# Optimization experiments

Hardware: AMD Instinct MI355X
Metric: run time of the kernel (lower is better)

Reference implementation:

```python
import jax, jax.numpy as jnp
import numpy as np

VOCAB, EMB, HID, T, B, NCLS = 50000, 300, 512, 128, 256, 3


def _lstm_final_h(x, lens, W, b):
    """TF BasicLSTMCell semantics (gate order i,j,f,o; forget_bias=1.0) with
    dynamic_rnn sequence_length masking; returns final hidden state [B, HID].
    x: [B, T, EMB] float, lens: [B] int, W: [EMB+HID, 4*HID], b: [4*HID].
    """
    xt = jnp.swapaxes(x, 0, 1)                       # [T, B, EMB]
    mask = jnp.arange(T)[:, None] < lens[None, :]    # [T, B]

    def step(carry, inp):
        c, h = carry
        x_t, m = inp
        z = jnp.concatenate([x_t, h], axis=-1) @ W + b   # [B, 4*HID]
        i, j, f, o = jnp.split(z, 4, axis=-1)
        c_new = c * jax.nn.sigmoid(f + 1.0) + jax.nn.sigmoid(i) * jnp.tanh(j)
        h_new = jnp.tanh(c_new) * jax.nn.sigmoid(o)
        m = m[:, None]
        return (jnp.where(m, c_new, c), jnp.where(m, h_new, h)), None

    init = (jnp.zeros((x.shape[0], HID), x.dtype),
            jnp.zeros((x.shape[0], HID), x.dtype))
    (c, h), _ = jax.lax.scan(step, init, (xt, mask))
    return h


def setup_inputs() -> dict:
    key = jax.random.key(0)
    ks = jax.random.split(key, 12)
    s = 0.05
    return {
        "left_ids": jax.random.randint(ks[0], (B, T), 0, VOCAB, dtype=jnp.int32),
        "right_ids": jax.random.randint(ks[1], (B, T), 0, VOCAB, dtype=jnp.int32),
        "left_len": jax.random.randint(ks[2], (B,), 1, T + 1, dtype=jnp.int32),
        "right_len": jax.random.randint(ks[3], (B,), 1, T + 1, dtype=jnp.int32),
        "embeddings": jax.random.normal(ks[4], (VOCAB, EMB), jnp.float32) * s,
        "W_l": jax.random.normal(ks[5], (EMB + HID, 4 * HID), jnp.float32) * s,
        "b_l": jnp.zeros((4 * HID,), jnp.float32),
        "W_r": jax.random.normal(ks[6], (EMB + HID, 4 * HID), jnp.float32) * s,
        "b_r": jnp.zeros((4 * HID,), jnp.float32),
        "W_d": jax.random.normal(ks[7], (2 * HID, NCLS), jnp.float32) * s,
        "b_d": jnp.zeros((NCLS,), jnp.float32),
    }


def reference(left_ids, right_ids, left_len, right_len,
              embeddings, W_l, b_l, W_r, b_r, W_d, b_d):
    left_x = embeddings[left_ids]      # [B, T, EMB]
    right_x = embeddings[right_ids]    # [B, T, EMB]
    h_l = _lstm_final_h(left_x, left_len, W_l, b_l)     # [B, HID]
    h_r = _lstm_final_h(right_x, right_len, W_r, b_r)   # [B, HID]
    logits = jnp.concatenate([h_l, h_r], axis=1) @ W_d + b_d  # [B, NCLS]
    return logits
```

## Files before the change

### kernel.cpp

```cpp
#include <hip/hip_runtime.h>


using bf16x8 = __attribute__((ext_vector_type(8))) __bf16;
using f32x4  = __attribute__((ext_vector_type(4))) float;
using u32x4  = __attribute__((ext_vector_type(4))) unsigned int;
typedef unsigned short u16;
typedef unsigned long long u64;

#define NT 128
#define ROWB 1664
#define SWZ(row, off) ((off) ^ (((row) & 7) << 4))

#define LGKM0  asm volatile("s_waitcnt lgkmcnt(0)" ::: "memory")
#define VM0    asm volatile("s_waitcnt vmcnt(0)" ::: "memory")
#define BAR()  __builtin_amdgcn_s_barrier()
#define SCHED0 __builtin_amdgcn_sched_barrier(0)

__device__ __forceinline__ u16 f2bf(float f) {
  union { float f; unsigned u; } v; v.f = f;
  unsigned r = v.u + 0x7fffu + ((v.u >> 16) & 1u);
  return (u16)(r >> 16);
}
__device__ __forceinline__ float sigf(float x) { return 1.f / (1.f + __expf(-x)); }
__device__ __forceinline__ float tanhf_(float x) { return 2.f / (1.f + __expf(-2.f * x)) - 1.f; }

__device__ __forceinline__ void setA26(bf16x8 (&A)[26], int kt, bf16x8 v) {
  switch (kt) {
    case 0:A[0]=v;break;  case 1:A[1]=v;break;  case 2:A[2]=v;break;
    case 3:A[3]=v;break;  case 4:A[4]=v;break;  case 5:A[5]=v;break;
    case 6:A[6]=v;break;  case 7:A[7]=v;break;  case 8:A[8]=v;break;
    case 9:A[9]=v;break;  case 10:A[10]=v;break; case 11:A[11]=v;break;
    case 12:A[12]=v;break; case 13:A[13]=v;break; case 14:A[14]=v;break;
    case 15:A[15]=v;break; case 16:A[16]=v;break; case 17:A[17]=v;break;
    case 18:A[18]=v;break; case 19:A[19]=v;break; case 20:A[20]=v;break;
    case 21:A[21]=v;break; case 22:A[22]=v;break; case 23:A[23]=v;break;
    case 24:A[24]=v;break; case 25:A[25]=v;break;
  }
}

__global__ __launch_bounds__(256, 1) void lstm_persist(
    const int* __restrict__ lids, const int* __restrict__ rids,
    const int* __restrict__ llen, const int* __restrict__ rlen,
    const float* __restrict__ emb,
    const float* __restrict__ Wl, const float* __restrict__ bl,
    const float* __restrict__ Wr, const float* __restrict__ br,
    u64* __restrict__ hbuf,
    float* __restrict__ hfin,
    unsigned int* __restrict__ bar)
{
  __shared__ __align__(16) unsigned char sB[32 * ROWB];
  __shared__ __align__(8)  u16 sH[32][36];
  __shared__ int sI[4096];

  const int tid = threadIdx.x;
  const int w = tid >> 6, l = tid & 63;
  const int bid = blockIdx.x;
  const int xcd = bid & 7, idx = bid >> 3;
  const int grp = xcd * 2 + (idx >> 4);
  const int ct  = idx & 15;
  const int lstm = grp >> 3, bt = grp & 7;
  const int b0 = bt * 32, u0 = ct * 32;

  const int*   ids  = lstm ? rids : lids;
  const int*   lenp = lstm ? rlen : llen;
  const float* W    = lstm ? Wr : Wl;
  const float* bv   = lstm ? br : bl;

  bf16x8 A0[26], A1[26];
  {
    float* sW = (float*)sB;
    for (int kc = 0; kc < 13; ++kc) {
      for (int i = 0; i < 32; ++i) {
        int id2 = tid + i * 256;
        int c = id2 & 31, r = (id2 >> 5) & 63, g = id2 >> 11;
        int kk = kc * 64 + r;
        float v = 0.f;
        if (kk < 300)       v = W[kk * 2048 + g * 512 + u0 + c];
        else if (kk >= 320) v = W[(kk - 20) * 2048 + g * 512 + u0 + c];
        sW[(g * 64 + r) * 32 + c] = v;
      }
      __syncthreads();
      #pragma unroll
      for (int kt2 = 0; kt2 < 2; ++kt2) {
        int kt = kc * 2 + kt2;
        #pragma unroll
        for (int mf2 = 0; mf2 < 2; ++mf2) {
          int mf = w * 2 + mf2;
          int rho = mf * 16 + (l & 15);
          int du = rho >> 2, g = rho & 3;
          union { u16 s[8]; bf16x8 v; } tmp;
          #pragma unroll
          for (int j = 0; j < 8; ++j) {
            int kr = kt2 * 32 + ((l >> 4) << 3) + j;
            tmp.s[j] = f2bf(sW[(g * 64 + kr) * 32 + du]);
          }
          if (mf2 == 0) setA26(A0, kt, tmp.v); else setA26(A1, kt, tmp.v);
        }
      }
      __syncthreads();
    }
  }

  if (tid < 160) {
    int row = tid / 5, c5 = tid - (tid / 5) * 5;
    *(u64*)(sB + row * ROWB + SWZ(row, 600 + c5 * 8)) = 0ULL;
  }
  {
    const int* src = ids + b0 * NT;
    #pragma unroll
    for (int i = 0; i < 4; ++i)
      *(int4*)&sI[(tid + i * 256) * 4] = *(const int4*)&src[(tid + i * 256) * 4];
  }
  __syncthreads();

  int ldsoff[10], sirow[10], foff[10];
  #pragma unroll
  for (int i = 0; i < 10; ++i) {
    int id2 = tid + i * 256;
    int row = id2 / 75, f4 = id2 - row * 75;
    ldsoff[i] = row * ROWB + SWZ(row, f4 * 8);
    sirow[i]  = row * NT;
    foff[i]   = f4 * 4;
  }
  int hoff[16];
  #pragma unroll
  for (int i = 0; i < 16; ++i) {
    int id2 = tid + i * 256;
    int row = id2 >> 7, c8 = id2 & 127;
    hoff[i] = row * ROWB + SWZ(row, 640 + c8 * 8);
  }

  int lenn[2];
  lenn[0] = lenp[b0 + (l & 15)];
  lenn[1] = lenp[b0 + 16 + (l & 15)];
  float bia[2][4];
  #pragma unroll
  for (int mf2 = 0; mf2 < 2; ++mf2) {
    int du = w * 8 + mf2 * 4 + (l >> 4);
    #pragma unroll
    for (int g = 0; g < 4; ++g) bia[mf2][g] = bv[g * 512 + u0 + du];
  }
  float cst[2][2] = {{0.f, 0.f}, {0.f, 0.f}};
  float hst[2][2] = {{0.f, 0.f}, {0.f, 0.f}};

  float4 px[10];
  #pragma unroll
  for (int i = 0; i < 10; ++i)
    if (i < 9 || tid < 96) {
      int eid = sI[sirow[i]];
      px[i] = *(const float4*)(emb + eid * 300 + foff[i]);
    }

  const int r0 = l & 15, r1 = 16 + (l & 15);

  for (int t = 0; t < NT; ++t) {
    u64 hld[16];
    const u64* hsrc = hbuf + (((lstm * 2 + ((t & 1) ^ 1)) * 256) + b0) * 128;
    #pragma unroll
    for (int i = 0; i < 16; ++i) {
      u64 v = 0ULL;
      if (t > 0)
        v = __hip_atomic_load(&hsrc[tid + i * 256], __ATOMIC_RELAXED,
                              __HIP_MEMORY_SCOPE_AGENT);
      hld[i] = v;
    }
    #pragma unroll
    for (int i = 0; i < 10; ++i)
      if (i < 9 || tid < 96) {
        float4 xv = px[i];
        u64 pk = (u64)f2bf(xv.x) | ((u64)f2bf(xv.y) << 16) |
                 ((u64)f2bf(xv.z) << 32) | ((u64)f2bf(xv.w) << 48);
        *(u64*)(sB + ldsoff[i]) = pk;
      }
    {
      int tn = (t + 1) & (NT - 1);
      #pragma unroll
      for (int i = 0; i < 10; ++i)
        if (i < 9 || tid < 96) {
          int eid = sI[sirow[i] + tn];
          px[i] = *(const float4*)(emb + eid * 300 + foff[i]);
        }
    }
    #pragma unroll
    for (int i = 0; i < 16; ++i) *(u64*)(sB + hoff[i]) = hld[i];

    LGKM0; BAR(); SCHED0;

    f32x4 acc[2][2];
    acc[0][0] = {0.f,0.f,0.f,0.f}; acc[0][1] = {0.f,0.f,0.f,0.f};
    acc[1][0] = {0.f,0.f,0.f,0.f}; acc[1][1] = {0.f,0.f,0.f,0.f};
    #pragma unroll
    for (int kt = 0; kt < 26; ++kt) {
      int kb = kt * 64 + ((l >> 4) << 4);
      bf16x8 B0 = __builtin_bit_cast(bf16x8, *(const u32x4*)(sB + r0 * ROWB + SWZ(r0, kb)));
      bf16x8 B1 = __builtin_bit_cast(bf16x8, *(const u32x4*)(sB + r1 * ROWB + SWZ(r1, kb)));
      acc[0][0] = __builtin_amdgcn_mfma_f32_16x16x32_bf16(A0[kt], B0, acc[0][0], 0, 0, 0);
      acc[0][1] = __builtin_amdgcn_mfma_f32_16x16x32_bf16(A0[kt], B1, acc[0][1], 0, 0, 0);
      acc[1][0] = __builtin_amdgcn_mfma_f32_16x16x32_bf16(A1[kt], B0, acc[1][0], 0, 0, 0);
      acc[1][1] = __builtin_amdgcn_mfma_f32_16x16x32_bf16(A1[kt], B1, acc[1][1], 0, 0, 0);
    }

    #pragma unroll
    for (int mf2 = 0; mf2 < 2; ++mf2)
      #pragma unroll
      for (int n = 0; n < 2; ++n) {
        f32x4 z = acc[mf2][n];
        float zi = z[0] + bia[mf2][0];
        float zj = z[1] + bia[mf2][1];
        float zf = z[2] + bia[mf2][2];
        float zo = z[3] + bia[mf2][3];
        float cn = cst[mf2][n] * sigf(zf + 1.f) + sigf(zi) * tanhf_(zj);
        float hn = tanhf_(cn) * sigf(zo);
        if (t < lenn[n]) { cst[mf2][n] = cn; hst[mf2][n] = hn; }
        sH[n * 16 + (l & 15)][w * 8 + mf2 * 4 + (l >> 4)] = f2bf(hst[mf2][n]);
      }
    LGKM0; BAR(); SCHED0;

    {
      int bbL = tid >> 3, u8 = tid & 7;
      u64 pk = *(const u64*)&sH[bbL][u8 * 4];
      u64* hdst = hbuf + (((lstm * 2 + (t & 1)) * 256) + b0 + bbL) * 128 + (u0 >> 2) + u8;
      __hip_atomic_store(hdst, pk, __ATOMIC_RELAXED, __HIP_MEMORY_SCOPE_AGENT);
    }
    VM0; BAR();

    if (tid == 0) {
      __hip_atomic_fetch_add(&bar[grp * 32], 1u, __ATOMIC_RELAXED,
                             __HIP_MEMORY_SCOPE_AGENT);
      unsigned target = 16u * (unsigned)(t + 1);
      while (__hip_atomic_load(&bar[grp * 32], __ATOMIC_RELAXED,
                               __HIP_MEMORY_SCOPE_AGENT) < target)
        __builtin_amdgcn_s_sleep(1);
    }
    BAR(); SCHED0;
  }

  #pragma unroll
  for (int mf2 = 0; mf2 < 2; ++mf2)
    #pragma unroll
    for (int n = 0; n < 2; ++n) {
      int bb = b0 + n * 16 + (l & 15);
      int uu = u0 + w * 8 + mf2 * 4 + (l >> 4);
      hfin[lstm * (256 * 512) + bb * 512 + uu] = hst[mf2][n];
    }
}

__global__ void dense_out(const float* __restrict__ hfin,
                          const float* __restrict__ Wd, const float* __restrict__ bd,
                          float* __restrict__ out) {
  const int b = blockIdx.x, l = threadIdx.x;
  float a0 = 0.f, a1 = 0.f, a2 = 0.f;
  for (int i = l; i < 1024; i += 64) {
    float hv = (i < 512) ? hfin[b * 512 + i] : hfin[256 * 512 + b * 512 + (i - 512)];
    a0 += hv * Wd[i * 3 + 0];
    a1 += hv * Wd[i * 3 + 1];
    a2 += hv * Wd[i * 3 + 2];
  }
  #pragma unroll
  for (int off = 32; off > 0; off >>= 1) {
    a0 += __shfl_down(a0, off);
    a1 += __shfl_down(a1, off);
    a2 += __shfl_down(a2, off);
  }
  if (l == 0) {
    out[b * 3 + 0] = a0 + bd[0];
    out[b * 3 + 1] = a1 + bd[1];
    out[b * 3 + 2] = a2 + bd[2];
  }
}

extern "C" void kernel_launch(void* const* d_in, const int* in_sizes, int n_in,
                              void* d_out, int out_size, void* d_ws, size_t ws_size,
                              hipStream_t stream) {
  const int*   lids = (const int*)d_in[0];
  const int*   rids = (const int*)d_in[1];
  const int*   llen = (const int*)d_in[2];
  const int*   rlen = (const int*)d_in[3];
  const float* emb  = (const float*)d_in[4];
  const float* Wl   = (const float*)d_in[5];
  const float* bl   = (const float*)d_in[6];
  const float* Wr   = (const float*)d_in[7];
  const float* br   = (const float*)d_in[8];
  const float* Wd   = (const float*)d_in[9];
  const float* bd   = (const float*)d_in[10];

  unsigned char* ws = (unsigned char*)d_ws;
  unsigned int* bar = (unsigned int*)ws;
  u64*   hbuf = (u64*)(ws + 4096);
  float* hfin = (float*)(ws + 4096 + (1u << 20));

  hipMemsetAsync(bar, 0, 2048, stream);
  hipLaunchKernelGGL(lstm_persist, dim3(256), dim3(256), 0, stream,
                     lids, rids, llen, rlen, emb, Wl, bl, Wr, br, hbuf, hfin, bar);
  hipLaunchKernelGGL(dense_out, dim3(256), dim3(64), 0, stream,
                     hfin, Wd, bd, (float*)d_out);
}
```

Baseline: 718.7 us.

## Overlap input-projection MFMAs with cross-block barrier wait in LSTM recurrence

Splits the per-step gate GEMM into the input part (k-tiles 0-9) and the recurrent part (k-tiles 10-25). After publishing h and signalling the inter-block counter, each block computes the next step's input contribution and prefetches embeddings two steps ahead, and only then waits on the barrier. This moves x-projection work and the embedding staging off the serial critical path between steps. It skips the h load and recurrent MFMAs at t=0, and splits the barrier into an arrive after the store and a wait at the start of the next step, which needs careful ordering of the LDS reuse of the x region.

```diff
diff --git a/kernel.cpp b/kernel.cpp
--- a/kernel.cpp
+++ b/kernel.cpp
@@ -65,6 +65,7 @@
   const int*   lenp = lstm ? rlen : llen;
   const float* W    = lstm ? Wr : Wl;
   const float* bv   = lstm ? br : bl;
+  unsigned int* const blp = bar + grp * 32;
 
   bf16x8 A0[26], A1[26];
   {
@@ -111,7 +112,6 @@
     for (int i = 0; i < 4; ++i)
       *(int4*)&sI[(tid + i * 256) * 4] = *(const int4*)&src[(tid + i * 256) * 4];
   }
-  __syncthreads();
 
   int ldsoff[10], sirow[10], foff[10];
   #pragma unroll
@@ -142,69 +142,76 @@
   }
   float cst[2][2] = {{0.f, 0.f}, {0.f, 0.f}};
   float hst[2][2] = {{0.f, 0.f}, {0.f, 0.f}};
+  __syncthreads();
 
   float4 px[10];
   #pragma unroll
   for (int i = 0; i < 10; ++i)
     if (i < 9 || tid < 96) {
       int eid = sI[sirow[i]];
+      float4 xv = *(const float4*)(emb + eid * 300 + foff[i]);
+      u64 pk = (u64)f2bf(xv.x) | ((u64)f2bf(xv.y) << 16) |
+               ((u64)f2bf(xv.z) << 32) | ((u64)f2bf(xv.w) << 48);
+      *(u64*)(sB + ldsoff[i]) = pk;
+    }
+  #pragma unroll
+  for (int i = 0; i < 10; ++i)
+    if (i < 9 || tid < 96) {
+      int eid = sI[sirow[i] + 1];
       px[i] = *(const float4*)(emb + eid * 300 + foff[i]);
     }
+  __syncthreads();
 
   const int r0 = l & 15, r1 = 16 + (l & 15);
 
+  f32x4 xacc[2][2];
+  xacc[0][0] = {0.f,0.f,0.f,0.f}; xacc[0][1] = {0.f,0.f,0.f,0.f};
+  xacc[1][0] = {0.f,0.f,0.f,0.f}; xacc[1][1] = {0.f,0.f,0.f,0.f};
+  #pragma unroll
+  for (int kt = 0; kt < 10; ++kt) {
+    int kb = kt * 64 + ((l >> 4) << 4);
+    bf16x8 B0 = __builtin_bit_cast(bf16x8, *(const u32x4*)(sB + r0 * ROWB + SWZ(r0, kb)));
+    bf16x8 B1 = __builtin_bit_cast(bf16x8, *(const u32x4*)(sB + r1 * ROWB + SWZ(r1, kb)));
+    xacc[0][0] = __builtin_amdgcn_mfma_f32_16x16x32_bf16(A0[kt], B0, xacc[0][0], 0, 0, 0);
+    xacc[0][1] = __builtin_amdgcn_mfma_f32_16x16x32_bf16(A0[kt], B1, xacc[0][1], 0, 0, 0);
+    xacc[1][0] = __builtin_amdgcn_mfma_f32_16x16x32_bf16(A1[kt], B0, xacc[1][0], 0, 0, 0);
+    xacc[1][1] = __builtin_amdgcn_mfma_f32_16x16x32_bf16(A1[kt], B1, xacc[1][1], 0, 0, 0);
+  }
+
   for (int t = 0; t < NT; ++t) {
-    u64 hld[16];
-    const u64* hsrc = hbuf + (((lstm * 2 + ((t & 1) ^ 1)) * 256) + b0) * 128;
-    #pragma unroll
-    for (int i = 0; i < 16; ++i) {
-      u64 v = 0ULL;
-      if (t > 0)
-        v = __hip_atomic_load(&hsrc[tid + i * 256], __ATOMIC_RELAXED,
-                              __HIP_MEMORY_SCOPE_AGENT);
-      hld[i] = v;
-    }
-    #pragma unroll
-    for (int i = 0; i < 10; ++i)
-      if (i < 9 || tid < 96) {
-        float4 xv = px[i];
-        u64 pk = (u64)f2bf(xv.x) | ((u64)f2bf(xv.y) << 16) |
-                 ((u64)f2bf(xv.z) << 32) | ((u64)f2bf(xv.w) << 48);
-        *(u64*)(sB + ldsoff[i]) = pk;
-      }
-    {
-      int tn = (t + 1) & (NT - 1);
-      #pragma unroll
-      for (int i = 0; i < 10; ++i)
-        if (i < 9 || tid < 96) {
-          int eid = sI[sirow[i] + tn];
-          px[i] = *(const float4*)(emb + eid * 300 + foff[i]);
-        }
-    }
-    #pragma unroll
-    for (int i = 0; i < 16; ++i) *(u64*)(sB + hoff[i]) = hld[i];
-
-    LGKM0; BAR(); SCHED0;
-
-    f32x4 acc[2][2];
-    acc[0][0] = {0.f,0.f,0.f,0.f}; acc[0][1] = {0.f,0.f,0.f,0.f};
-    acc[1][0] = {0.f,0.f,0.f,0.f}; acc[1][1] = {0.f,0.f,0.f,0.f};
-    #pragma unroll
-    for (int kt = 0; kt < 26; ++kt) {
-      int kb = kt * 64 + ((l >> 4) << 4);
-      bf16x8 B0 = __builtin_bit_cast(bf16x8, *(const u32x4*)(sB + r0 * ROWB + SWZ(r0, kb)));
-      bf16x8 B1 = __builtin_bit_cast(bf16x8, *(const u32x4*)(sB + r1 * ROWB + SWZ(r1, kb)));
-      acc[0][0] = __builtin_amdgcn_mfma_f32_16x16x32_bf16(A0[kt], B0, acc[0][0], 0, 0, 0);
-      acc[0][1] = __builtin_amdgcn_mfma_f32_16x16x32_bf16(A0[kt], B1, acc[0][1], 0, 0, 0);
-      acc[1][0] = __builtin_amdgcn_mfma_f32_16x16x32_bf16(A1[kt], B0, acc[1][0], 0, 0, 0);
-      acc[1][1] = __builtin_amdgcn_mfma_f32_16x16x32_bf16(A1[kt], B1, acc[1][1], 0, 0, 0);
+    if (t > 0) {
+      if (tid == 0) {
+        unsigned target = 16u * (unsigned)t;
+        while (__hip_atomic_load(blp, __ATOMIC_RELAXED, __HIP_MEMORY_SCOPE_AGENT) < target)
+          __builtin_amdgcn_s_sleep(1);
+      }
+      BAR(); SCHED0;
+      const u64* hsrc = hbuf + (((lstm * 2 + ((t & 1) ^ 1)) * 256) + b0) * 128;
+      u64 hld[16];
+      #pragma unroll
+      for (int i = 0; i < 16; ++i)
+        hld[i] = __hip_atomic_load(&hsrc[tid + i * 256], __ATOMIC_RELAXED,
+                                   __HIP_MEMORY_SCOPE_AGENT);
+      #pragma unroll
+      for (int i = 0; i < 16; ++i) *(u64*)(sB + hoff[i]) = hld[i];
+      LGKM0; BAR(); SCHED0;
+      #pragma unroll
+      for (int kt = 10; kt < 26; ++kt) {
+        int kb = kt * 64 + ((l >> 4) << 4);
+        bf16x8 B0 = __builtin_bit_cast(bf16x8, *(const u32x4*)(sB + r0 * ROWB + SWZ(r0, kb)));
+        bf16x8 B1 = __builtin_bit_cast(bf16x8, *(const u32x4*)(sB + r1 * ROWB + SWZ(r1, kb)));
+        xacc[0][0] = __builtin_amdgcn_mfma_f32_16x16x32_bf16(A0[kt], B0, xacc[0][0], 0, 0, 0);
+        xacc[0][1] = __builtin_amdgcn_mfma_f32_16x16x32_bf16(A0[kt], B1, xacc[0][1], 0, 0, 0);
+        xacc[1][0] = __builtin_amdgcn_mfma_f32_16x16x32_bf16(A1[kt], B0, xacc[1][0], 0, 0, 0);
+        xacc[1][1] = __builtin_amdgcn_mfma_f32_16x16x32_bf16(A1[kt], B1, xacc[1][1], 0, 0, 0);
+      }
     }
 
     #pragma unroll
     for (int mf2 = 0; mf2 < 2; ++mf2)
       #pragma unroll
       for (int n = 0; n < 2; ++n) {
-        f32x4 z = acc[mf2][n];
+        f32x4 z = xacc[mf2][n];
         float zi = z[0] + bia[mf2][0];
         float zj = z[1] + bia[mf2][1];
         float zf = z[2] + bia[mf2][2];
@@ -222,17 +229,41 @@
       u64* hdst = hbuf + (((lstm * 2 + (t & 1)) * 256) + b0 + bbL) * 128 + (u0 >> 2) + u8;
       __hip_atomic_store(hdst, pk, __ATOMIC_RELAXED, __HIP_MEMORY_SCOPE_AGENT);
     }
-    VM0; BAR();
-
-    if (tid == 0) {
-      __hip_atomic_fetch_add(&bar[grp * 32], 1u, __ATOMIC_RELAXED,
-                             __HIP_MEMORY_SCOPE_AGENT);
-      unsigned target = 16u * (unsigned)(t + 1);
-      while (__hip_atomic_load(&bar[grp * 32], __ATOMIC_RELAXED,
-                               __HIP_MEMORY_SCOPE_AGENT) < target)
-        __builtin_amdgcn_s_sleep(1);
-    }
-    BAR(); SCHED0;
+    #pragma unroll
+    for (int i = 0; i < 10; ++i)
+      if (i < 9 || tid < 96) {
+        float4 xv = px[i];
+        u64 pk = (u64)f2bf(xv.x) | ((u64)f2bf(xv.y) << 16) |
+                 ((u64)f2bf(xv.z) << 32) | ((u64)f2bf(xv.w) << 48);
+        *(u64*)(sB + ldsoff[i]) = pk;
+      }
+    VM0; LGKM0; BAR();
+
+    if (tid == 0)
+      __hip_atomic_fetch_add(blp, 1u, __ATOMIC_RELAXED, __HIP_MEMORY_SCOPE_AGENT);
+    SCHED0;
+
+    {
+      int tn2 = (t + 2) & (NT - 1);
+      #pragma unroll
+      for (int i = 0; i < 10; ++i)
+        if (i < 9 || tid < 96) {
+          int eid = sI[sirow[i] + tn2];
+          px[i] = *(const float4*)(emb + eid * 300 + foff[i]);
+        }
+    }
+    xacc[0][0] = {0.f,0.f,0.f,0.f}; xacc[0][1] = {0.f,0.f,0.f,0.f};
+    xacc[1][0] = {0.f,0.f,0.f,0.f}; xacc[1][1] = {0.f,0.f,0.f,0.f};
+    #pragma unroll
+    for (int kt = 0; kt < 10; ++kt) {
+      int kb = kt * 64 + ((l >> 4) << 4);
+      bf16x8 B0 = __builtin_bit_cast(bf16x8, *(const u32x4*)(sB + r0 * ROWB + SWZ(r0, kb)));
+      bf16x8 B1 = __builtin_bit_cast(bf16x8, *(const u32x4*)(sB + r1 * ROWB + SWZ(r1, kb)));
+      xacc[0][0] = __builtin_amdgcn_mfma_f32_16x16x32_bf16(A0[kt], B0, xacc[0][0], 0, 0, 0);
+      xacc[0][1] = __builtin_amdgcn_mfma_f32_16x16x32_bf16(A0[kt], B1, xacc[0][1], 0, 0, 0);
+      xacc[1][0] = __builtin_amdgcn_mfma_f32_16x16x32_bf16(A1[kt], B0, xacc[1][0], 0, 0, 0);
+      xacc[1][1] = __builtin_amdgcn_mfma_f32_16x16x32_bf16(A1[kt], B1, xacc[1][1], 0, 0, 0);
+    }
   }
 
   #pragma unroll
```

Result: faster. 667.9 us (-7.1%).

## Interleave left and right LSTMs per block to overlap sync with input GEMM

Applied to the files above, without the earlier changes.

Each block now owns a 16-unit column slice of both LSTMs instead of a 32-unit slice of one, holding both weight sets in registers. Per timestep it alternates between the left and right recurrence, splitting the barrier into a separate arrive and a later wait. While one LSTM's cross-block barrier is pending, the block runs the other LSTM's input-projection MFMAs and embedding gathers. This hides the global-barrier latency, at the cost of more barriers per block, more blocks per barrier group (32 instead of 16), and a larger LDS footprint. Token ids are now read straight from global memory rather than staged in LDS.

```diff
diff --git a/kernel.cpp b/kernel.cpp
--- a/kernel.cpp
+++ b/kernel.cpp
@@ -8,7 +8,8 @@
 typedef unsigned long long u64;
 
 #define NT 128
-#define ROWB 1664
+#define ROWB 2304
+#define X1B  1664
 #define SWZ(row, off) ((off) ^ (((row) & 7) << 4))
 
 #define LGKM0  asm volatile("s_waitcnt lgkmcnt(0)" ::: "memory")
@@ -20,6 +21,10 @@
   union { float f; unsigned u; } v; v.f = f;
   unsigned r = v.u + 0x7fffu + ((v.u >> 16) & 1u);
   return (u16)(r >> 16);
+}
+__device__ __forceinline__ u64 pack4(float4 xv) {
+  return (u64)f2bf(xv.x) | ((u64)f2bf(xv.y) << 16) |
+         ((u64)f2bf(xv.z) << 32) | ((u64)f2bf(xv.w) << 48);
 }
 __device__ __forceinline__ float sigf(float x) { return 1.f / (1.f + __expf(-x)); }
 __device__ __forceinline__ float tanhf_(float x) { return 2.f / (1.f + __expf(-2.f * x)) - 1.f; }
@@ -38,6 +43,60 @@
   }
 }
 
+__device__ __forceinline__ void buildA(bf16x8 (&A)[26], const float* __restrict__ W,
+                                       float* sW, int tid, int l, int w, int u0) {
+  for (int kc = 0; kc < 13; ++kc) {
+    for (int i = 0; i < 16; ++i) {
+      int id2 = tid + i * 256;
+      int c = id2 & 15, r = (id2 >> 4) & 63, g = id2 >> 10;
+      int kk = kc * 64 + r;
+      float v = 0.f;
+      if (kk < 300)       v = W[kk * 2048 + g * 512 + u0 + c];
+      else if (kk >= 320) v = W[(kk - 20) * 2048 + g * 512 + u0 + c];
+      sW[(g * 64 + r) * 16 + c] = v;
+    }
+    __syncthreads();
+    #pragma unroll
+    for (int kt2 = 0; kt2 < 2; ++kt2) {
+      int rho = w * 16 + (l & 15);
+      int du = rho >> 2, g = rho & 3;
+      union { u16 s[8]; bf16x8 v; } tmp;
+      #pragma unroll
+      for (int j = 0; j < 8; ++j) {
+        int kr = kt2 * 32 + ((l >> 4) << 3) + j;
+        tmp.s[j] = f2bf(sW[(g * 64 + kr) * 16 + du]);
+      }
+      setA26(A, kc * 2 + kt2, tmp.v);
+    }
+    __syncthreads();
+  }
+}
+
+__device__ __forceinline__ void xgemm10(f32x4 (&acc)[2], const bf16x8 (&A)[26],
+                                        const unsigned char* sB, int l, int xb) {
+  const int r0 = l & 15, r1 = 16 + (l & 15);
+  #pragma unroll
+  for (int kt = 0; kt < 10; ++kt) {
+    int kb = xb + kt * 64 + ((l >> 4) << 4);
+    bf16x8 B0 = __builtin_bit_cast(bf16x8, *(const u32x4*)(sB + r0 * ROWB + SWZ(r0, kb)));
+    bf16x8 B1 = __builtin_bit_cast(bf16x8, *(const u32x4*)(sB + r1 * ROWB + SWZ(r1, kb)));
+    acc[0] = __builtin_amdgcn_mfma_f32_16x16x32_bf16(A[kt], B0, acc[0], 0, 0, 0);
+    acc[1] = __builtin_amdgcn_mfma_f32_16x16x32_bf16(A[kt], B1, acc[1], 0, 0, 0);
+  }
+}
+__device__ __forceinline__ void hgemm16(f32x4 (&acc)[2], const bf16x8 (&A)[26],
+                                        const unsigned char* sB, int l) {
+  const int r0 = l & 15, r1 = 16 + (l & 15);
+  #pragma unroll
+  for (int kt = 10; kt < 26; ++kt) {
+    int kb = kt * 64 + ((l >> 4) << 4);
+    bf16x8 B0 = __builtin_bit_cast(bf16x8, *(const u32x4*)(sB + r0 * ROWB + SWZ(r0, kb)));
+    bf16x8 B1 = __builtin_bit_cast(bf16x8, *(const u32x4*)(sB + r1 * ROWB + SWZ(r1, kb)));
+    acc[0] = __builtin_amdgcn_mfma_f32_16x16x32_bf16(A[kt], B0, acc[0], 0, 0, 0);
+    acc[1] = __builtin_amdgcn_mfma_f32_16x16x32_bf16(A[kt], B1, acc[1], 0, 0, 0);
+  }
+}
+
 __global__ __launch_bounds__(256, 1) void lstm_persist(
     const int* __restrict__ lids, const int* __restrict__ rids,
     const int* __restrict__ llen, const int* __restrict__ rlen,
@@ -49,200 +108,202 @@
     unsigned int* __restrict__ bar)
 {
   __shared__ __align__(16) unsigned char sB[32 * ROWB];
-  __shared__ __align__(8)  u16 sH[32][36];
-  __shared__ int sI[4096];
+  __shared__ __align__(8)  u16 sH[32][20];
 
   const int tid = threadIdx.x;
   const int w = tid >> 6, l = tid & 63;
   const int bid = blockIdx.x;
-  const int xcd = bid & 7, idx = bid >> 3;
-  const int grp = xcd * 2 + (idx >> 4);
-  const int ct  = idx & 15;
-  const int lstm = grp >> 3, bt = grp & 7;
-  const int b0 = bt * 32, u0 = ct * 32;
-
-  const int*   ids  = lstm ? rids : lids;
-  const int*   lenp = lstm ? rlen : llen;
-  const float* W    = lstm ? Wr : Wl;
-  const float* bv   = lstm ? br : bl;
+  const int bt = bid >> 5, ct = bid & 31;
+  const int b0 = bt * 32, u0 = ct * 16;
+
+  unsigned int* const c0 = bar + bt * 32;
+  unsigned int* const c1 = bar + (8 + bt) * 32;
 
   bf16x8 A0[26], A1[26];
-  {
-    float* sW = (float*)sB;
-    for (int kc = 0; kc < 13; ++kc) {
-      for (int i = 0; i < 32; ++i) {
-        int id2 = tid + i * 256;
-        int c = id2 & 31, r = (id2 >> 5) & 63, g = id2 >> 11;
-        int kk = kc * 64 + r;
-        float v = 0.f;
-        if (kk < 300)       v = W[kk * 2048 + g * 512 + u0 + c];
-        else if (kk >= 320) v = W[(kk - 20) * 2048 + g * 512 + u0 + c];
-        sW[(g * 64 + r) * 32 + c] = v;
-      }
-      __syncthreads();
-      #pragma unroll
-      for (int kt2 = 0; kt2 < 2; ++kt2) {
-        int kt = kc * 2 + kt2;
-        #pragma unroll
-        for (int mf2 = 0; mf2 < 2; ++mf2) {
-          int mf = w * 2 + mf2;
-          int rho = mf * 16 + (l & 15);
-          int du = rho >> 2, g = rho & 3;
-          union { u16 s[8]; bf16x8 v; } tmp;
-          #pragma unroll
-          for (int j = 0; j < 8; ++j) {
-            int kr = kt2 * 32 + ((l >> 4) << 3) + j;
-            tmp.s[j] = f2bf(sW[(g * 64 + kr) * 32 + du]);
-          }
-          if (mf2 == 0) setA26(A0, kt, tmp.v); else setA26(A1, kt, tmp.v);
-        }
-      }
-      __syncthreads();
-    }
-  }
+  buildA(A0, Wl, (float*)sB, tid, l, w, u0);
+  buildA(A1, Wr, (float*)sB, tid, l, w, u0);
 
   if (tid < 160) {
     int row = tid / 5, c5 = tid - (tid / 5) * 5;
     *(u64*)(sB + row * ROWB + SWZ(row, 600 + c5 * 8)) = 0ULL;
-  }
-  {
-    const int* src = ids + b0 * NT;
-    #pragma unroll
-    for (int i = 0; i < 4; ++i)
-      *(int4*)&sI[(tid + i * 256) * 4] = *(const int4*)&src[(tid + i * 256) * 4];
-  }
-  __syncthreads();
-
-  int ldsoff[10], sirow[10], foff[10];
+    *(u64*)(sB + row * ROWB + SWZ(row, 2264 + c5 * 8)) = 0ULL;
+  }
+
+  int xrow[10], xf4[10];
   #pragma unroll
   for (int i = 0; i < 10; ++i) {
     int id2 = tid + i * 256;
-    int row = id2 / 75, f4 = id2 - row * 75;
-    ldsoff[i] = row * ROWB + SWZ(row, f4 * 8);
-    sirow[i]  = row * NT;
-    foff[i]   = f4 * 4;
+    int row = (id2 < 2400) ? id2 / 75 : 0;
+    xrow[i] = row;
+    xf4[i]  = id2 - row * 75;
   }
   int hoff[16];
   #pragma unroll
   for (int i = 0; i < 16; ++i) {
-    int id2 = tid + i * 256;
-    int row = id2 >> 7, c8 = id2 & 127;
+    int idx = tid + i * 256;
+    int row = idx >> 7, c8 = idx & 127;
     hoff[i] = row * ROWB + SWZ(row, 640 + c8 * 8);
   }
 
-  int lenn[2];
-  lenn[0] = lenp[b0 + (l & 15)];
-  lenn[1] = lenp[b0 + 16 + (l & 15)];
-  float bia[2][4];
-  #pragma unroll
-  for (int mf2 = 0; mf2 < 2; ++mf2) {
-    int du = w * 8 + mf2 * 4 + (l >> 4);
-    #pragma unroll
-    for (int g = 0; g < 4; ++g) bia[mf2][g] = bv[g * 512 + u0 + du];
-  }
-  float cst[2][2] = {{0.f, 0.f}, {0.f, 0.f}};
-  float hst[2][2] = {{0.f, 0.f}, {0.f, 0.f}};
-
-  float4 px[10];
+  const int du = w * 4 + (l >> 4);
+  int lenn0[2], lenn1[2];
+  #pragma unroll
+  for (int n = 0; n < 2; ++n) {
+    lenn0[n] = llen[b0 + n * 16 + (l & 15)];
+    lenn1[n] = rlen[b0 + n * 16 + (l & 15)];
+  }
+  float bia0[4], bia1[4];
+  #pragma unroll
+  for (int g = 0; g < 4; ++g) {
+    bia0[g] = bl[g * 512 + u0 + du];
+    bia1[g] = br[g * 512 + u0 + du];
+  }
+  float cst0[2] = {0.f, 0.f}, hst0[2] = {0.f, 0.f};
+  float cst1[2] = {0.f, 0.f}, hst1[2] = {0.f, 0.f};
+  __syncthreads();
+
   #pragma unroll
   for (int i = 0; i < 10; ++i)
     if (i < 9 || tid < 96) {
-      int eid = sI[sirow[i]];
-      px[i] = *(const float4*)(emb + eid * 300 + foff[i]);
-    }
-
-  const int r0 = l & 15, r1 = 16 + (l & 15);
+      int eid = lids[(b0 + xrow[i]) * NT];
+      float4 xv = *(const float4*)(emb + eid * 300 + xf4[i] * 4);
+      *(u64*)(sB + xrow[i] * ROWB + SWZ(xrow[i], xf4[i] * 8)) = pack4(xv);
+    }
+  __syncthreads();
 
   for (int t = 0; t < NT; ++t) {
-    u64 hld[16];
-    const u64* hsrc = hbuf + (((lstm * 2 + ((t & 1) ^ 1)) * 256) + b0) * 128;
-    #pragma unroll
-    for (int i = 0; i < 16; ++i) {
-      u64 v = 0ULL;
-      if (t > 0)
-        v = __hip_atomic_load(&hsrc[tid + i * 256], __ATOMIC_RELAXED,
-                              __HIP_MEMORY_SCOPE_AGENT);
-      hld[i] = v;
-    }
-    #pragma unroll
-    for (int i = 0; i < 10; ++i)
-      if (i < 9 || tid < 96) {
-        float4 xv = px[i];
-        u64 pk = (u64)f2bf(xv.x) | ((u64)f2bf(xv.y) << 16) |
-                 ((u64)f2bf(xv.z) << 32) | ((u64)f2bf(xv.w) << 48);
-        *(u64*)(sB + ldsoff[i]) = pk;
-      }
+    if (t > 0) {
+      if (tid == 0) {
+        unsigned target = 32u * (unsigned)t;
+        while (__hip_atomic_load(c0, __ATOMIC_RELAXED, __HIP_MEMORY_SCOPE_AGENT) < target)
+          __builtin_amdgcn_s_sleep(1);
+      }
+      BAR(); SCHED0;
+    }
+    {
+      int eidv[10];
+      #pragma unroll
+      for (int i = 0; i < 10; ++i)
+        if (i < 9 || tid < 96) eidv[i] = rids[(b0 + xrow[i]) * NT + t];
+      u64 hld[16];
+      if (t > 0) {
+        const u64* hsrc = hbuf + ((((t & 1) ^ 1)) * 256 + b0) * 128;
+        #pragma unroll
+        for (int i = 0; i < 16; ++i)
+          hld[i] = __hip_atomic_load(&hsrc[tid + i * 256], __ATOMIC_RELAXED,
+                                     __HIP_MEMORY_SCOPE_AGENT);
+      }
+      f32x4 acc[2];
+      acc[0] = {0.f,0.f,0.f,0.f}; acc[1] = {0.f,0.f,0.f,0.f};
+      xgemm10(acc, A0, sB, l, 0);
+      float4 xg[10];
+      #pragma unroll
+      for (int i = 0; i < 10; ++i)
+        if (i < 9 || tid < 96)
+          xg[i] = *(const float4*)(emb + eidv[i] * 300 + xf4[i] * 4);
+      if (t > 0) {
+        #pragma unroll
+        for (int i = 0; i < 16; ++i) *(u64*)(sB + hoff[i]) = hld[i];
+        LGKM0; BAR(); SCHED0;
+        hgemm16(acc, A0, sB, l);
+      }
+      #pragma unroll
+      for (int n = 0; n < 2; ++n) {
+        f32x4 z = acc[n];
+        float zi = z[0] + bia0[0], zj = z[1] + bia0[1];
+        float zf = z[2] + bia0[2], zo = z[3] + bia0[3];
+        float cn = cst0[n] * sigf(zf + 1.f) + sigf(zi) * tanhf_(zj);
+        float hn = tanhf_(cn) * sigf(zo);
+        if (t < lenn0[n]) { cst0[n] = cn; hst0[n] = hn; }
+        sH[n * 16 + (l & 15)][du] = f2bf(hst0[n]);
+      }
+      LGKM0; BAR(); SCHED0;
+      if (tid < 128) {
+        int row = tid >> 2, q = tid & 3;
+        u64 pk = *(const u64*)&sH[row][q * 4];
+        u64* hdst = hbuf + (((t & 1)) * 256 + b0 + row) * 128 + ct * 4 + q;
+        __hip_atomic_store(hdst, pk, __ATOMIC_RELAXED, __HIP_MEMORY_SCOPE_AGENT);
+      }
+      #pragma unroll
+      for (int i = 0; i < 10; ++i)
+        if (i < 9 || tid < 96)
+          *(u64*)(sB + xrow[i] * ROWB + SWZ(xrow[i], X1B + xf4[i] * 8)) = pack4(xg[i]);
+      VM0; LGKM0; BAR();
+      if (tid == 0)
+        __hip_atomic_fetch_add(c0, 1u, __ATOMIC_RELAXED, __HIP_MEMORY_SCOPE_AGENT);
+      SCHED0;
+    }
+
+    if (t > 0) {
+      if (tid == 0) {
+        unsigned target = 32u * (unsigned)t;
+        while (__hip_atomic_load(c1, __ATOMIC_RELAXED, __HIP_MEMORY_SCOPE_AGENT) < target)
+          __builtin_amdgcn_s_sleep(1);
+      }
+      BAR(); SCHED0;
+    }
     {
       int tn = (t + 1) & (NT - 1);
-      #pragma unroll
-      for (int i = 0; i < 10; ++i)
-        if (i < 9 || tid < 96) {
-          int eid = sI[sirow[i] + tn];
-          px[i] = *(const float4*)(emb + eid * 300 + foff[i]);
-        }
-    }
-    #pragma unroll
-    for (int i = 0; i < 16; ++i) *(u64*)(sB + hoff[i]) = hld[i];
-
-    LGKM0; BAR(); SCHED0;
-
-    f32x4 acc[2][2];
-    acc[0][0] = {0.f,0.f,0.f,0.f}; acc[0][1] = {0.f,0.f,0.f,0.f};
-    acc[1][0] = {0.f,0.f,0.f,0.f}; acc[1][1] = {0.f,0.f,0.f,0.f};
-    #pragma unroll
-    for (int kt = 0; kt < 26; ++kt) {
-      int kb = kt * 64 + ((l >> 4) << 4);
-      bf16x8 B0 = __builtin_bit_cast(bf16x8, *(const u32x4*)(sB + r0 * ROWB + SWZ(r0, kb)));
-      bf16x8 B1 = __builtin_bit_cast(bf16x8, *(const u32x4*)(sB + r1 * ROWB + SWZ(r1, kb)));
-      acc[0][0] = __builtin_amdgcn_mfma_f32_16x16x32_bf16(A0[kt], B0, acc[0][0], 0, 0, 0);
-      acc[0][1] = __builtin_amdgcn_mfma_f32_16x16x32_bf16(A0[kt], B1, acc[0][1], 0, 0, 0);
-      acc[1][0] = __builtin_amdgcn_mfma_f32_16x16x32_bf16(A1[kt], B0, acc[1][0], 0, 0, 0);
-      acc[1][1] = __builtin_amdgcn_mfma_f32_16x16x32_bf16(A1[kt], B1, acc[1][1], 0, 0, 0);
-    }
-
-    #pragma unroll
-    for (int mf2 = 0; mf2 < 2; ++mf2)
+      int eidv[10];
+      #pragma unroll
+      for (int i = 0; i < 10; ++i)
+        if (i < 9 || tid < 96) eidv[i] = lids[(b0 + xrow[i]) * NT + tn];
+      u64 hld[16];
+      if (t > 0) {
+        const u64* hsrc = hbuf + ((2 + ((t & 1) ^ 1)) * 256 + b0) * 128;
+        #pragma unroll
+        for (int i = 0; i < 16; ++i)
+          hld[i] = __hip_atomic_load(&hsrc[tid + i * 256], __ATOMIC_RELAXED,
+                                     __HIP_MEMORY_SCOPE_AGENT);
+      }
+      f32x4 acc[2];
+      acc[0] = {0.f,0.f,0.f,0.f}; acc[1] = {0.f,0.f,0.f,0.f};
+      xgemm10(acc, A1, sB, l, X1B);
+      float4 xg[10];
+      #pragma unroll
+      for (int i = 0; i < 10; ++i)
+        if (i < 9 || tid < 96)
+          xg[i] = *(const float4*)(emb + eidv[i] * 300 + xf4[i] * 4);
+      if (t > 0) {
+        #pragma unroll
+        for (int i = 0; i < 16; ++i) *(u64*)(sB + hoff[i]) = hld[i];
+        LGKM0; BAR(); SCHED0;
+        hgemm16(acc, A1, sB, l);
+      }
       #pragma unroll
       for (int n = 0; n < 2; ++n) {
-        f32x4 z = acc[mf2][n];
-        float zi = z[0] + bia[mf2][0];
-        float zj = z[1] + bia[mf2][1];
-        float zf = z[2] + bia[mf2][2];
-        float zo = z[3] + bia[mf2][3];
-        float cn = cst[mf2][n] * sigf(zf + 1.f) + sigf(zi) * tanhf_(zj);
+        f32x4 z = acc[n];
+        float zi = z[0] + bia1[0], zj = z[1] + bia1[1];
+        float zf = z[2] + bia1[2], zo = z[3] + bia1[3];
+        float cn = cst1[n] * sigf(zf + 1.f) + sigf(zi) * tanhf_(zj);
         float hn = tanhf_(cn) * sigf(zo);
-        if (t < lenn[n]) { cst[mf2][n] = cn; hst[mf2][n] = hn; }
-        sH[n * 16 + (l & 15)][w * 8 + mf2 * 4 + (l >> 4)] = f2bf(hst[mf2][n]);
-      }
-    LGKM0; BAR(); SCHED0;
-
-    {
-      int bbL = tid >> 3, u8 = tid & 7;
-      u64 pk = *(const u64*)&sH[bbL][u8 * 4];
-      u64* hdst = hbuf + (((lstm * 2 + (t & 1)) * 256) + b0 + bbL) * 128 + (u0 >> 2) + u8;
-      __hip_atomic_store(hdst, pk, __ATOMIC_RELAXED, __HIP_MEMORY_SCOPE_AGENT);
-    }
-    VM0; BAR();
-
-    if (tid == 0) {
-      __hip_atomic_fetch_add(&bar[grp * 32], 1u, __ATOMIC_RELAXED,
-                             __HIP_MEMORY_SCOPE_AGENT);
-      unsigned target = 16u * (unsigned)(t + 1);
-      while (__hip_atomic_load(&bar[grp * 32], __ATOMIC_RELAXED,
-                               __HIP_MEMORY_SCOPE_AGENT) < target)
-        __builtin_amdgcn_s_sleep(1);
-    }
-    BAR(); SCHED0;
-  }
-
-  #pragma unroll
-  for (int mf2 = 0; mf2 < 2; ++mf2)
-    #pragma unroll
-    for (int n = 0; n < 2; ++n) {
-      int bb = b0 + n * 16 + (l & 15);
-      int uu = u0 + w * 8 + mf2 * 4 + (l >> 4);
-      hfin[lstm * (256 * 512) + bb * 512 + uu] = hst[mf2][n];
-    }
+        if (t < lenn1[n]) { cst1[n] = cn; hst1[n] = hn; }
+        sH[n * 16 + (l & 15)][du] = f2bf(hst1[n]);
+      }
+      LGKM0; BAR(); SCHED0;
+      if (tid < 128) {
+        int row = tid >> 2, q = tid & 3;
+        u64 pk = *(const u64*)&sH[row][q * 4];
+        u64* hdst = hbuf + ((2 + (t & 1)) * 256 + b0 + row) * 128 + ct * 4 + q;
+        __hip_atomic_store(hdst, pk, __ATOMIC_RELAXED, __HIP_MEMORY_SCOPE_AGENT);
+      }
+      #pragma unroll
+      for (int i = 0; i < 10; ++i)
+        if (i < 9 || tid < 96)
+          *(u64*)(sB + xrow[i] * ROWB + SWZ(xrow[i], xf4[i] * 8)) = pack4(xg[i]);
+      VM0; LGKM0; BAR();
+      if (tid == 0)
+        __hip_atomic_fetch_add(c1, 1u, __ATOMIC_RELAXED, __HIP_MEMORY_SCOPE_AGENT);
+      SCHED0;
+    }
+  }
+
+  #pragma unroll
+  for (int n = 0; n < 2; ++n) {
+    int bb = b0 + n * 16 + (l & 15);
+    hfin[bb * 512 + u0 + du] = hst0[n];
+    hfin[256 * 512 + bb * 512 + u0 + du] = hst1[n];
+  }
 }
 
 __global__ void dense_out(const float* __restrict__ hfin,
```

Measured after the change: 1.106 ms. +53.9%, slower.
